# Performance work log

Measured on AMD Instinct MI355X. Metric: run time of the kernel, lower is better.

Reference implementation:

```python
import jax, jax.numpy as jnp
import numpy as np
from jax import lax

B = 8192      # batch (many parallel RL envs)
E = 16        # token_embed_size
IE = 128      # image_embed_size == semi_memory_size == LSTM hidden
H = 128       # text GRU hidden (text_embedding_size)
W_EMB = 32    # word_embedding_size
T = 20        # text length
V = 100       # text vocab (obs_space['text'])
NACT = 7      # action_space.n
EMB = IE + H  # embedding_size = 256


def setup_inputs() -> dict:
    key = jax.random.key(0)
    ks = jax.random.split(key, 32)
    f = lambda k, shape, s=0.1: (jax.random.normal(k, shape, jnp.float32) * s)
    C1 = IE // 2
    return {
        'image': jax.random.randint(ks[0], (B, 7, 7, 3), 0, 2),
        'memory': jax.random.normal(ks[1], (B, 2 * IE), jnp.float32),
        'text': jax.random.randint(ks[2], (B, T), 0, V),
        'obj_emb': f(ks[3], (11, E)),
        'col_emb': f(ks[4], (6, E)),
        'st_emb': f(ks[5], (2, E)),
        'conv1_w': f(ks[6], (C1, 3 * E, 2, 2)), 'conv1_b': jnp.zeros((C1,), jnp.float32),
        'conv2_w': f(ks[7], (C1, C1, 2, 2)), 'conv2_b': jnp.zeros((C1,), jnp.float32),
        'conv3_w': f(ks[8], (IE, C1, 2, 2)), 'conv3_b': jnp.zeros((IE,), jnp.float32),
        'lstm_wih': f(ks[9], (4 * IE, IE)), 'lstm_whh': f(ks[10], (4 * IE, IE)),
        'lstm_bih': jnp.zeros((4 * IE,), jnp.float32), 'lstm_bhh': jnp.zeros((4 * IE,), jnp.float32),
        'word_emb': f(ks[11], (V, W_EMB)),
        'gru_wih': f(ks[12], (3 * H, W_EMB)), 'gru_whh': f(ks[13], (3 * H, H)),
        'gru_bih': jnp.zeros((3 * H,), jnp.float32), 'gru_bhh': jnp.zeros((3 * H,), jnp.float32),
        'actor_w1': f(ks[14], (EMB, EMB)), 'actor_b1': jnp.zeros((EMB,), jnp.float32),
        'actor_w2': f(ks[15], (NACT, EMB)), 'actor_b2': jnp.zeros((NACT,), jnp.float32),
        'critic_w1': f(ks[16], (EMB, EMB)), 'critic_b1': jnp.zeros((EMB,), jnp.float32),
        'critic_w2': f(ks[17], (1, EMB)), 'critic_b2': jnp.zeros((1,), jnp.float32),
    }


def reference(image, memory, text, obj_emb, col_emb, st_emb,
              conv1_w, conv1_b, conv2_w, conv2_b, conv3_w, conv3_b,
              lstm_wih, lstm_whh, lstm_bih, lstm_bhh,
              word_emb, gru_wih, gru_whh, gru_bih, gru_bhh,
              actor_w1, actor_b1, actor_w2, actor_b2,
              critic_w1, critic_b1, critic_w2, critic_b2):
    Hs = lstm_whh.shape[1]
    # embed + concat (color, object, state) on last dim, then NHWC->NCHW
    im = jnp.concatenate([col_emb[image[..., 1]], obj_emb[image[..., 0]], st_emb[image[..., 2]]], axis=3)
    x = jnp.transpose(im, (0, 3, 1, 2))  # [B, 3E, 7, 7]
    dn = ('NCHW', 'OIHW', 'NCHW')
    conv = lambda x, w, b: lax.conv_general_dilated(x, w, (1, 1), 'VALID', dimension_numbers=dn) + b[None, :, None, None]
    x = jax.nn.relu(conv(x, conv1_w, conv1_b))                                 # [B, 64, 6, 6]
    x = lax.reduce_window(x, -jnp.inf, lax.max, (1, 1, 2, 2), (1, 1, 2, 2), 'VALID')  # [B, 64, 3, 3]
    x = jax.nn.relu(conv(x, conv2_w, conv2_b))                                 # [B, 64, 2, 2]
    x = jax.nn.relu(conv(x, conv3_w, conv3_b))                                 # [B, 128, 1, 1]
    x = x.reshape(x.shape[0], -1)
    # LSTMCell (torch gate order i, f, g, o)
    h, c = memory[:, :Hs], memory[:, Hs:]
    gates = x @ lstm_wih.T + lstm_bih + h @ lstm_whh.T + lstm_bhh
    i, f, g, o = jnp.split(gates, 4, axis=1)
    c = jax.nn.sigmoid(f) * c + jax.nn.sigmoid(i) * jnp.tanh(g)
    h = jax.nn.sigmoid(o) * jnp.tanh(c)
    memory_out = jnp.concatenate([h, c], axis=1)
    # text GRU (torch gate order r, z, n); precompute input-side gates
    wemb = word_emb[text]  # [B, T, 32]
    gi_all = jnp.einsum('btd,gd->btg', wemb, gru_wih) + gru_bih  # [B, T, 3H]
    HH = gru_whh.shape[1]
    def step(ht, gi):
        gh = ht @ gru_whh.T + gru_bhh
        r = jax.nn.sigmoid(gi[:, :HH] + gh[:, :HH])
        z = jax.nn.sigmoid(gi[:, HH:2 * HH] + gh[:, HH:2 * HH])
        n = jnp.tanh(gi[:, 2 * HH:] + r * gh[:, 2 * HH:])
        return (1.0 - z) * n + z * ht, None
    h0 = jnp.zeros((wemb.shape[0], HH), wemb.dtype)
    ht, _ = lax.scan(step, h0, jnp.swapaxes(gi_all, 0, 1))
    emb = jnp.concatenate([h, ht], axis=1)  # [B, 256]
    logits = jnp.tanh(emb @ actor_w1.T + actor_b1) @ actor_w2.T + actor_b2
    log_probs = jax.nn.log_softmax(logits, axis=1)  # Categorical logits
    value = (jnp.tanh(emb @ critic_w1.T + critic_b1) @ critic_w2.T + critic_b2)[:, 0]
    return (log_probs, value, memory_out)
```

## Files before the change

kernel.cpp:

```cpp
#include <hip/hip_runtime.h>

#define Bsz   8192
#define Tlen  20
#define OUT_VAL_OFF  57344
#define OUT_MEM_OFF  65536

#define WS_GI     0
#define WS_D1     153600
#define WS_WT     161792
#define WS_WHF    686080
#define WS_WTBH   882688
#define WS_WTBL   1144832
#define WS_LB     1406976
#define WS_C2W    1409024
#define WS_C2B    1474560
#define WS_C3W    1474816
#define WS_C3B    1605888
#define WS_C1B    1606400
#define WS_BH     1606656
#define WS_B1     1608192
#define WS_W2     1610240
#define WS_B2     1618432
#define WS_FLAG   1618464
#define WS_WHB    1618496
#define WS_LWTB   1716800

#define GBLK   512
#define GROWS  16
#define PREP_TASKS 404616

using frag16 = __attribute__((ext_vector_type(8))) short;
using fragf4 = __attribute__((ext_vector_type(4))) float;

__device__ __forceinline__ float bf2f(unsigned short u){
    union { unsigned int i; float f; } v; v.i = ((unsigned int)u) << 16; return v.f;
}
__device__ __forceinline__ unsigned short f2bf(float f){
    union { float f; unsigned int i; } v; v.f = f;
    unsigned int x = v.i;
    return (unsigned short)((x + 0x7fffu + ((x >> 16) & 1u)) >> 16);
}
__device__ __forceinline__ float sigm(float x){ return 1.0f / (1.0f + __expf(-x)); }
__device__ __forceinline__ float tanh_f(float x){ return 1.0f - 2.0f / (__expf(2.0f * x) + 1.0f); }

template<bool BF>
__device__ __forceinline__ float G(const void* p, int i){
    if (BF) return bf2f(((const unsigned short*)p)[i]);
    else    return ((const float*)p)[i];
}

__global__ __launch_bounds__(256) void sniff_kernel(
    const unsigned short* __restrict__ we, int* __restrict__ flag)
{
    __shared__ int cnt;
    if (threadIdx.x == 0) cnt = 0;
    __syncthreads();
    int c = 0;
    for (int i = threadIdx.x; i < 2048; i += 256) {
        int e = (we[i] >> 7) & 0xFF;
        if (e >= 96 && e <= 160) c++;
    }
    atomicAdd(&cnt, c);
    __syncthreads();
    if (threadIdx.x == 0) *flag = (cnt >= 1792) ? 1 : 0;
}

template<bool BF>
__global__ __launch_bounds__(256) void prep_kernel(
    const int* __restrict__ flag,
    const void* word_emb, const void* gru_wih, const void* gru_bih,
    const void* col_emb, const void* obj_emb, const void* st_emb,
    const void* conv1_w, const void* conv1_b,
    const void* conv2_w, const void* conv2_b,
    const void* conv3_w, const void* conv3_b,
    const void* lstm_wih, const void* lstm_whh,
    const void* lstm_bih, const void* lstm_bhh,
    const void* actor_w1, const void* actor_b1,
    const void* actor_w2, const void* actor_b2,
    const void* critic_w1, const void* critic_b1,
    const void* critic_w2, const void* critic_b2,
    const void* gru_whh, const void* gru_bhh,
    float* __restrict__ ws0)
{
    if ((*flag != 0) != BF) return;
    int task = blockIdx.x * 256 + threadIdx.x;
    if (task >= PREP_TASKS) return;
    char* wsb = (char*)ws0;
    if (task < 38400) {
        int v = task / 384, g = task - v * 384;
        float acc = G<BF>(gru_bih, g);
        #pragma unroll
        for (int d = 0; d < 32; d++)
            acc += G<BF>(word_emb, v * 32 + d) * G<BF>(gru_wih, g * 32 + d);
        ((float*)(wsb + WS_GI))[task] = acc;
    } else if (task < 40448) {
        int i2 = task - 38400;
        int o = i2 & 63; int tkk = i2 >> 6;
        int kx = tkk & 1, ky = (tkk >> 1) & 1, t = tkk >> 2;
        int c = t & 1, ob = (t >> 1) & 1, s = (t >> 2) & 1;
        float acc = 0.f;
        #pragma unroll
        for (int i = 0; i < 48; i++) {
            float e;
            if (i < 16)      e = G<BF>(col_emb, c * 16 + i);
            else if (i < 32) e = G<BF>(obj_emb, ob * 16 + (i - 16));
            else             e = G<BF>(st_emb, s * 16 + (i - 32));
            acc += e * G<BF>(conv1_w, ((o * 48 + i) * 2 + ky) * 2 + kx);
        }
        ((float*)(wsb + WS_D1))[tkk * 64 + ((o + tkk) & 63)] = acc;
    } else if (task < 171520) {
        int i3 = task - 40448;
        int u = i3 >> 8, k = i3 & 255;
        float w = (u < 256) ? G<BF>(actor_w1, u * 256 + k)
                            : G<BF>(critic_w1, (u - 256) * 256 + k);
        unsigned short hi = f2bf(w);
        ((unsigned short*)(wsb + WS_WTBH))[i3] = hi;
        ((unsigned short*)(wsb + WS_WTBL))[i3] = f2bf(w - bf2f(hi));
    } else if (task < 172032) {
        int i = task - 171520;
        ((float*)(wsb + WS_LB))[i] = G<BF>(lstm_bih, i) + G<BF>(lstm_bhh, i);
    } else if (task < 188416) {
        int i = task - 172032;
        int o = i & 63, pp = (i >> 6) & 3, ii = i >> 8;
        ((float*)(wsb + WS_C2W))[i] = G<BF>(conv2_w, o * 256 + ii * 4 + pp);
    } else if (task < 188480) {
        int i = task - 188416;
        ((float*)(wsb + WS_C2B))[i] = G<BF>(conv2_b, i);
    } else if (task < 221248) {
        int i = task - 188480;
        int o = i & 127, kk = i >> 7;
        ((float*)(wsb + WS_C3W))[i] = G<BF>(conv3_w, o * 256 + kk);
    } else if (task < 221376) {
        int i = task - 221248;
        ((float*)(wsb + WS_C3B))[i] = G<BF>(conv3_b, i);
    } else if (task < 221440) {
        int i = task - 221376;
        ((float*)(wsb + WS_C1B))[i] = G<BF>(conv1_b, i);
    } else if (task < 221824) {
        int i = task - 221440;
        ((float*)(wsb + WS_BH))[i] = G<BF>(gru_bhh, i);
    } else if (task < 222336) {
        int i = task - 221824;
        ((float*)(wsb + WS_B1))[i] = (i < 256) ? G<BF>(actor_b1, i) : G<BF>(critic_b1, i - 256);
    } else if (task < 224384) {
        int i = task - 222336;
        int u = i >> 8, k = i & 255;
        ((float*)(wsb + WS_W2))[i] = (u < 7) ? G<BF>(actor_w2, u * 256 + k) : G<BF>(critic_w2, k);
    } else if (task < 224392) {
        int i = task - 224384;
        ((float*)(wsb + WS_B2))[i] = (i < 7) ? G<BF>(actor_b2, i) : G<BF>(critic_b2, 0);
    } else if (task < 273544) {
        int i = task - 224392;
        ((unsigned short*)(wsb + WS_WHB))[i] = f2bf(G<BF>(gru_whh, i));
    } else {
        int i = task - 273544;
        int g = i >> 8, k = i & 255;
        float v = (k < 128) ? G<BF>(lstm_wih, g * 128 + k)
                            : G<BF>(lstm_whh, g * 128 + (k - 128));
        ((unsigned short*)(wsb + WS_LWTB))[i] = f2bf(v);
    }
}

__global__ __launch_bounds__(256) void conv_kernel(
    const int* __restrict__ image,
    const float* __restrict__ ws0,
    float* __restrict__ mem_out)
{
    const char* wsb = (const char*)ws0;
    const float* D1g  = (const float*)(wsb + WS_D1);
    const float* c1bF = (const float*)(wsb + WS_C1B);
    const float* c2wT = (const float*)(wsb + WS_C2W);
    const float* c2bF = (const float*)(wsb + WS_C2B);
    const float* c3wT = (const float*)(wsb + WS_C3W);
    const float* c3bF = (const float*)(wsb + WS_C3B);

    __shared__ __align__(16) float sp1[576 * 8];
    __shared__ __align__(16) float sp2[256 * 9];
    __shared__ __align__(16) float sD1[2048];
    __shared__ unsigned char stt[392];

    int tid = threadIdx.x;
    int b0 = blockIdx.x * 8;

    for (int i = tid; i < 2048; i += 256) sD1[i] = D1g[i];
    for (int i = tid; i < 392; i += 256) {
        int s = i / 49, p = i - s * 49;
        int base = ((b0 + s) * 49 + p) * 3;
        stt[i] = (unsigned char)(image[base + 1] | (image[base] << 1) | (image[base + 2] << 2));
    }
    __syncthreads();

    for (int task = tid; task < 4608; task += 256) {
        int s = task & 7;
        int op = task >> 3;
        int o = op / 9, p = op - o * 9;
        int py = p / 3, px = p - py * 3;
        float bo = c1bF[o];
        float mx = 0.f;
        #pragma unroll
        for (int dy = 0; dy < 2; dy++)
        #pragma unroll
        for (int dx = 0; dx < 2; dx++) {
            int y = 2 * py + dy, x = 2 * px + dx;
            float sum = bo;
            #pragma unroll
            for (int ky = 0; ky < 2; ky++)
            #pragma unroll
            for (int kx = 0; kx < 2; kx++) {
                int t = stt[s * 49 + (y + ky) * 7 + (x + kx)];
                int tkk = t * 4 + ky * 2 + kx;
                sum += sD1[tkk * 64 + ((o + tkk) & 63)];
            }
            mx = fmaxf(mx, sum);
        }
        sp1[op * 8 + s] = mx;
    }
    __syncthreads();

    {
        int ot = tid & 63, st4 = tid >> 6;
        int s0 = st4 * 2;
        float b = c2bF[ot];
        float acc[4][2];
        #pragma unroll
        for (int p = 0; p < 4; p++) { acc[p][0] = b; acc[p][1] = b; }
        for (int i = 0; i < 64; i++) {
            float w0 = c2wT[(i * 4 + 0) * 64 + ot];
            float w1 = c2wT[(i * 4 + 1) * 64 + ot];
            float w2 = c2wT[(i * 4 + 2) * 64 + ot];
            float w3 = c2wT[(i * 4 + 3) * 64 + ot];
            #pragma unroll
            for (int ss = 0; ss < 2; ss++) {
                const float* vr = sp1 + i * 72 + s0 + ss;
                float v0 = vr[0],  v1 = vr[8],  v2 = vr[16];
                float v3 = vr[24], v4 = vr[32], v5 = vr[40];
                float v6 = vr[48], v7 = vr[56], v8 = vr[64];
                acc[0][ss] += w0 * v0 + w1 * v1 + w2 * v3 + w3 * v4;
                acc[1][ss] += w0 * v1 + w1 * v2 + w2 * v4 + w3 * v5;
                acc[2][ss] += w0 * v3 + w1 * v4 + w2 * v6 + w3 * v7;
                acc[3][ss] += w0 * v4 + w1 * v5 + w2 * v7 + w3 * v8;
            }
        }
        int key = ot >> 3;
        #pragma unroll
        for (int p = 0; p < 4; p++)
            #pragma unroll
            for (int ss = 0; ss < 2; ss++)
                sp2[(ot * 4 + p) * 9 + ((s0 + ss + key) & 7)] = fmaxf(acc[p][ss], 0.f);
    }
    __syncthreads();

    {
        int ot = tid & 127, st2 = tid >> 7;
        int s0 = st2 * 4;
        float b = c3bF[ot];
        float acc[4] = { b, b, b, b };
        for (int kk = 0; kk < 256; kk++) {
            float w = c3wT[kk * 128 + ot];
            const float* ar = sp2 + kk * 9;
            int sw = (kk >> 5) & 7;
            acc[0] = fmaf(w, ar[(s0 + 0 + sw) & 7], acc[0]);
            acc[1] = fmaf(w, ar[(s0 + 1 + sw) & 7], acc[1]);
            acc[2] = fmaf(w, ar[(s0 + 2 + sw) & 7], acc[2]);
            acc[3] = fmaf(w, ar[(s0 + 3 + sw) & 7], acc[3]);
        }
        #pragma unroll
        for (int ss = 0; ss < 4; ss++)
            mem_out[(b0 + s0 + ss) * 256 + ot] = fmaxf(acc[ss], 0.f);
    }
}

#define GI_LOAD(dst, t) do {                                                  \
    _Pragma("unroll")                                                         \
    for (int rg_ = 0; rg_ < 4; rg_++) {                                       \
        int tok_ = sTok2[(m0 + rg_) * Tlen + (t)];                            \
        const float* gp_ = gi_table + tok_ * 384 + j;                         \
        dst[rg_ * 3 + 0] = gp_[0];                                            \
        dst[rg_ * 3 + 1] = gp_[128];                                          \
        dst[rg_ * 3 + 2] = gp_[256];                                          \
    }                                                                         \
} while (0)

#define GRU_STEP(SRD, SWR, GC, GN, T) do {                                    \
    frag16 Af_[4];                                                            \
    _Pragma("unroll")                                                         \
    for (int kc_ = 0; kc_ < 4; kc_++)                                         \
        Af_[kc_] = *(const frag16*)((SRD) + l16 * 136 + kc_ * 32 + quad * 8); \
    fragf4 aR_ = {0.f,0.f,0.f,0.f}, aZ_ = {0.f,0.f,0.f,0.f};                  \
    fragf4 aN_ = {0.f,0.f,0.f,0.f};                                           \
    _Pragma("unroll")                                                         \
    for (int kc_ = 0; kc_ < 4; kc_++) {                                       \
        aR_ = __builtin_amdgcn_mfma_f32_16x16x32_bf16(Af_[kc_], Bf0[kc_], aR_, 0, 0, 0); \
        aZ_ = __builtin_amdgcn_mfma_f32_16x16x32_bf16(Af_[kc_], Bf1[kc_], aZ_, 0, 0, 0); \
        aN_ = __builtin_amdgcn_mfma_f32_16x16x32_bf16(Af_[kc_], Bf2[kc_], aN_, 0, 0, 0); \
    }                                                                         \
    if ((T) < Tlen - 1) GI_LOAD(GN, (T) + 1);                                 \
    _Pragma("unroll")                                                         \
    for (int reg_ = 0; reg_ < 4; reg_++) {                                    \
        float rg2_ = sigm(GC[reg_*3+0] + aR_[reg_] + bh0);                    \
        float zg_  = sigm(GC[reg_*3+1] + aZ_[reg_] + bh1);                    \
        float ng_  = tanh_f(GC[reg_*3+2] + rg2_ * (aN_[reg_] + bh2));         \
        float hn_  = (1.f - zg_) * ng_ + zg_ * hpv[reg_];                     \
        unsigned short hb_ = f2bf(hn_);                                       \
        hpv[reg_] = bf2f(hb_);                                                \
        (SWR)[(m0 + reg_) * 136 + j] = hb_;                                   \
    }                                                                         \
    __syncthreads();                                                          \
} while (0)

__global__ __launch_bounds__(512, 4) void gru_head_kernel(
    const int* __restrict__ flag,
    const int* __restrict__ text, const void* memory,
    const float* __restrict__ ws0,
    float* __restrict__ mem_out,
    float* __restrict__ out_lp, float* __restrict__ out_val)
{
    const char* wsb = (const char*)ws0;
    const unsigned short* whb2 = (const unsigned short*)(wsb + WS_WHB);
    const unsigned short* lwtb = (const unsigned short*)(wsb + WS_LWTB);
    const unsigned short* wtbh = (const unsigned short*)(wsb + WS_WTBH);
    const unsigned short* wtbl = (const unsigned short*)(wsb + WS_WTBL);
    const float* gi_table = (const float*)(wsb + WS_GI);
    const float* bhF      = (const float*)(wsb + WS_BH);
    const float* b1F      = (const float*)(wsb + WS_B1);
    const float* W2f      = (const float*)(wsb + WS_W2);
    const float* B2f      = (const float*)(wsb + WS_B2);
    const float* lbF      = (const float*)(wsb + WS_LB);

    __shared__ __align__(16) char sU[25600];
    __shared__ float sScore[64];
    __shared__ int   sTok2[320];

    unsigned short* sEh  = (unsigned short*)sU;
    unsigned short* sEl  = (unsigned short*)(sU + 8448);
    unsigned short* sHtA = (unsigned short*)(sU + 16896);
    unsigned short* sHtB = (unsigned short*)(sU + 21248);
    float* sHid = (float*)sU;

    int tid = threadIdx.x;
    int rbase = blockIdx.x * GROWS;
    int wave = tid >> 6, lane = tid & 63;
    int quad = lane >> 4, l16 = lane & 15;
    int j = wave * 16 + l16;
    int m0 = quad * 4;
    const bool bfin = (*flag != 0);
    const unsigned short* mem16 = (const unsigned short*)memory;
    const float*          memf  = (const float*)memory;

    for (int i = tid; i < 4096; i += 512) {
        int m = i >> 8, k = i & 255;
        float v;
        if (k < 128) v = mem_out[(rbase + m) * 256 + k];
        else v = bfin ? bf2f(mem16[(rbase + m) * 256 + (k - 128)])
                      : memf[(rbase + m) * 256 + (k - 128)];
        sEh[m * 264 + k] = f2bf(v);
    }
    for (int i = tid; i < 2176; i += 512) sHtA[i] = 0;
    if (tid < 320) sTok2[tid] = text[rbase * Tlen + tid];
    __syncthreads();

    {
        frag16 Ax[8];
        #pragma unroll
        for (int kc = 0; kc < 8; kc++)
            Ax[kc] = *(const frag16*)(sEh + l16 * 264 + kc * 32 + quad * 8);
        fragf4 aI = {0.f,0.f,0.f,0.f}, aF = {0.f,0.f,0.f,0.f};
        fragf4 aG = {0.f,0.f,0.f,0.f}, aO = {0.f,0.f,0.f,0.f};
        #pragma unroll
        for (int kc = 0; kc < 8; kc++) {
            int ko = kc * 32 + quad * 8;
            frag16 bI = *(const frag16*)(lwtb + (j)       * 256 + ko);
            frag16 bF = *(const frag16*)(lwtb + (128 + j) * 256 + ko);
            frag16 bG = *(const frag16*)(lwtb + (256 + j) * 256 + ko);
            frag16 bO = *(const frag16*)(lwtb + (384 + j) * 256 + ko);
            aI = __builtin_amdgcn_mfma_f32_16x16x32_bf16(Ax[kc], bI, aI, 0, 0, 0);
            aF = __builtin_amdgcn_mfma_f32_16x16x32_bf16(Ax[kc], bF, aF, 0, 0, 0);
            aG = __builtin_amdgcn_mfma_f32_16x16x32_bf16(Ax[kc], bG, aG, 0, 0, 0);
            aO = __builtin_amdgcn_mfma_f32_16x16x32_bf16(Ax[kc], bO, aO, 0, 0, 0);
        }
        float lbI = lbF[j], lbFg = lbF[128 + j], lbG = lbF[256 + j], lbO = lbF[384 + j];
        __syncthreads();
        #pragma unroll
        for (int reg = 0; reg < 4; reg++) {
            int m = m0 + reg;
            float ig = sigm(aI[reg] + lbI);
            float fg = sigm(aF[reg] + lbFg);
            float gv = tanh_f(aG[reg] + lbG);
            float og = sigm(aO[reg] + lbO);
            float cv = bfin ? bf2f(mem16[(rbase + m) * 256 + 128 + j])
                            : memf[(rbase + m) * 256 + 128 + j];
            float cn = fg * cv + ig * gv;
            float hn = og * tanh_f(cn);
            mem_out[(rbase + m) * 256 + j]       = hn;
            mem_out[(rbase + m) * 256 + 128 + j] = cn;
            unsigned short hh = f2bf(hn);
            sEh[m * 264 + j] = hh;
            sEl[m * 264 + j] = f2bf(hn - bf2f(hh));
        }
    }

    frag16 Bf0[4], Bf1[4], Bf2[4];
    #pragma unroll
    for (int kc = 0; kc < 4; kc++) {
        int ko = kc * 32 + quad * 8;
        Bf0[kc] = *(const frag16*)(whb2 + (j)       * 128 + ko);
        Bf1[kc] = *(const frag16*)(whb2 + (128 + j) * 128 + ko);
        Bf2[kc] = *(const frag16*)(whb2 + (256 + j) * 128 + ko);
    }
    float bh0 = bhF[j], bh1 = bhF[128 + j], bh2 = bhF[256 + j];
    float hpv[4] = { 0.f, 0.f, 0.f, 0.f };
    float ga[12], gb[12];

    GI_LOAD(ga, 0);

    for (int tt = 0; tt < 10; tt++) {
        int t0 = tt * 2;
        GRU_STEP(sHtA, sHtB, ga, gb, t0);
        GRU_STEP(sHtB, sHtA, gb, ga, t0 + 1);
    }

    #pragma unroll
    for (int reg = 0; reg < 4; reg++) {
        int m = m0 + reg;
        sEh[m * 264 + 128 + j] = f2bf(hpv[reg]);
    }
    __syncthreads();

    fragf4 acc[4];
    {
        fragf4 z4 = {0.f,0.f,0.f,0.f};
        #pragma unroll
        for (int jb = 0; jb < 4; jb++) acc[jb] = z4;
        #pragma unroll
        for (int kc = 0; kc < 8; kc++) {
            int ko = kc * 32 + quad * 8;
            frag16 Eh = *(const frag16*)(sEh + l16 * 264 + ko);
            #pragma unroll
            for (int jb = 0; jb < 4; jb++) {
                int u = jb * 128 + wave * 16 + l16;
                frag16 Wh = *(const frag16*)(wtbh + u * 256 + ko);
                frag16 Wl = *(const frag16*)(wtbl + u * 256 + ko);
                acc[jb] = __builtin_amdgcn_mfma_f32_16x16x32_bf16(Eh, Wh, acc[jb], 0, 0, 0);
                acc[jb] = __builtin_amdgcn_mfma_f32_16x16x32_bf16(Eh, Wl, acc[jb], 0, 0, 0);
            }
            if (kc < 4) {
                frag16 El = *(const frag16*)(sEl + l16 * 264 + ko);
                #pragma unroll
                for (int jb = 0; jb < 4; jb++) {
                    int u = jb * 128 + wave * 16 + l16;
                    frag16 Wh = *(const frag16*)(wtbh + u * 256 + ko);
                    acc[jb] = __builtin_amdgcn_mfma_f32_16x16x32_bf16(El, Wh, acc[jb], 0, 0, 0);
                }
            }
        }
    }
    __syncthreads();

    #pragma unroll
    for (int half = 0; half < 2; half++) {
        if ((quad >> 1) == half) {
            #pragma unroll
            for (int jb = 0; jb < 4; jb++) {
                int u = jb * 128 + wave * 16 + l16;
                float bu = b1F[u];
                #pragma unroll
                for (int reg = 0; reg < 4; reg++) {
                    int mm = (m0 & 7) + reg;
                    sHid[u * 8 + ((mm + (u & 7)) & 7)] = tanh_f(acc[jb][reg] + bu);
                }
            }
        }
        __syncthreads();
        float acc2 = 0.f;
        int r = tid >> 3, i = tid & 7;
        if (tid < 64) {
            acc2 = B2f[i];
            const float* wrp = W2f + i * 256;
            int ubase = (i < 7) ? 0 : 256;
            for (int k = 0; k < 256; k++) {
                int u = ubase + k;
                acc2 += wrp[k] * sHid[u * 8 + ((r + (u & 7)) & 7)];
            }
            sScore[tid] = acc2;
        }
        __syncthreads();
        if (tid < 64) {
            const float* sr = sScore + r * 8;
            float mx = sr[0];
            #pragma unroll
            for (int a = 1; a < 7; a++) mx = fmaxf(mx, sr[a]);
            float se = 0.f;
            #pragma unroll
            for (int a = 0; a < 7; a++) se += __expf(sr[a] - mx);
            float lse = mx + __logf(se);
            int row = rbase + half * 8 + r;
            if (i < 7) out_lp[row * 7 + i] = acc2 - lse;
            else       out_val[row] = acc2;
        }
        if (half == 0) __syncthreads();
    }
}

extern "C" void kernel_launch(void* const* d_in, const int* in_sizes, int n_in,
                              void* d_out, int out_size, void* d_ws, size_t ws_size,
                              hipStream_t stream) {
    const int*  image  = (const int*)d_in[0];
    const void* memory = d_in[1];
    const int*  text   = (const int*)d_in[2];

    char* wsb = (char*)d_ws;
    float* ws0  = (float*)wsb;
    int*   flag = (int*)(wsb + WS_FLAG);

    float* out = (float*)d_out;
    float* out_lp  = out;
    float* out_val = out + OUT_VAL_OFF;
    float* mem_out = out + OUT_MEM_OFF;

    sniff_kernel<<<1, 256, 0, stream>>>((const unsigned short*)d_in[16], flag);

    const int PREP_GRID = (PREP_TASKS + 255) / 256;
    prep_kernel<true><<<PREP_GRID, 256, 0, stream>>>(flag,
        d_in[16], d_in[17], d_in[19], d_in[4], d_in[3], d_in[5],
        d_in[6], d_in[7], d_in[8], d_in[9], d_in[10], d_in[11],
        d_in[12], d_in[13], d_in[14], d_in[15],
        d_in[21], d_in[22], d_in[23], d_in[24],
        d_in[25], d_in[26], d_in[27], d_in[28],
        d_in[18], d_in[20], ws0);
    prep_kernel<false><<<PREP_GRID, 256, 0, stream>>>(flag,
        d_in[16], d_in[17], d_in[19], d_in[4], d_in[3], d_in[5],
        d_in[6], d_in[7], d_in[8], d_in[9], d_in[10], d_in[11],
        d_in[12], d_in[13], d_in[14], d_in[15],
        d_in[21], d_in[22], d_in[23], d_in[24],
        d_in[25], d_in[26], d_in[27], d_in[28],
        d_in[18], d_in[20], ws0);

    conv_kernel<<<Bsz / 8, 256, 0, stream>>>(image, ws0, mem_out);

    gru_head_kernel<<<GBLK, 512, 0, stream>>>(flag, text, memory, ws0,
                                              mem_out, out_lp, out_val);
}
```

Baseline: 279.9 us.

## Move conv2 and conv3 to bf16x3 split-precision MFMA

Conv2 and conv3 in the conv kernel now run on MFMA 16x16x32 bf16 instructions instead of scalar FP32 FMA loops. Activations and weights are split into high and low bf16 parts, and three MFMAs per tile keep accuracy close to FP32. A prep step writes the split weights into the workspace. The conv stages should become much cheaper, but the kernel does more MFMAs than a plain bf16 version and conv3 leaves half its M tile idle because there are only 8 samples per block.

Measured after the change: 266.9 us. 4.6% less time.

```diff
diff --git a/kernel.cpp b/kernel.cpp
--- a/kernel.cpp
+++ b/kernel.cpp
@@ -7,7 +7,10 @@
 
 #define WS_GI     0
 #define WS_D1     153600
-#define WS_WT     161792
+#define WS_W2BH   161792
+#define WS_W2BL   194560
+#define WS_W3BH   227328
+#define WS_W3BL   292864
 #define WS_WHF    686080
 #define WS_WTBH   882688
 #define WS_WTBL   1144832
@@ -27,7 +30,7 @@
 
 #define GBLK   512
 #define GROWS  16
-#define PREP_TASKS 404616
+#define PREP_TASKS 453768
 
 using frag16 = __attribute__((ext_vector_type(8))) short;
 using fragf4 = __attribute__((ext_vector_type(4))) float;
@@ -39,6 +42,12 @@
     union { float f; unsigned int i; } v; v.f = f;
     unsigned int x = v.i;
     return (unsigned short)((x + 0x7fffu + ((x >> 16) & 1u)) >> 16);
+}
+__device__ __forceinline__ void f2bf2(float f, unsigned short &h, unsigned short &l){
+    union { float f; unsigned int i; } u; u.f = f;
+    h = (unsigned short)(u.i >> 16);
+    union { unsigned int i; float f; } t; t.i = u.i & 0xffff0000u;
+    l = f2bf(f - t.f);
 }
 __device__ __forceinline__ float sigm(float x){ return 1.0f / (1.0f + __expf(-x)); }
 __device__ __forceinline__ float tanh_f(float x){ return 1.0f - 2.0f / (__expf(2.0f * x) + 1.0f); }
@@ -152,12 +161,24 @@
     } else if (task < 273544) {
         int i = task - 224392;
         ((unsigned short*)(wsb + WS_WHB))[i] = f2bf(G<BF>(gru_whh, i));
-    } else {
+    } else if (task < 404616) {
         int i = task - 273544;
         int g = i >> 8, k = i & 255;
         float v = (k < 128) ? G<BF>(lstm_wih, g * 128 + k)
                             : G<BF>(lstm_whh, g * 128 + (k - 128));
         ((unsigned short*)(wsb + WS_LWTB))[i] = f2bf(v);
+    } else if (task < 421000) {
+        int i = task - 404616;
+        float w = G<BF>(conv2_w, i);
+        unsigned short hi = f2bf(w);
+        ((unsigned short*)(wsb + WS_W2BH))[i] = hi;
+        ((unsigned short*)(wsb + WS_W2BL))[i] = f2bf(w - bf2f(hi));
+    } else {
+        int i = task - 421000;
+        float w = G<BF>(conv3_w, i);
+        unsigned short hi = f2bf(w);
+        ((unsigned short*)(wsb + WS_W3BH))[i] = hi;
+        ((unsigned short*)(wsb + WS_W3BL))[i] = f2bf(w - bf2f(hi));
     }
 }
 
@@ -169,18 +190,24 @@
     const char* wsb = (const char*)ws0;
     const float* D1g  = (const float*)(wsb + WS_D1);
     const float* c1bF = (const float*)(wsb + WS_C1B);
-    const float* c2wT = (const float*)(wsb + WS_C2W);
     const float* c2bF = (const float*)(wsb + WS_C2B);
-    const float* c3wT = (const float*)(wsb + WS_C3W);
     const float* c3bF = (const float*)(wsb + WS_C3B);
-
-    __shared__ __align__(16) float sp1[576 * 8];
-    __shared__ __align__(16) float sp2[256 * 9];
+    const unsigned short* w2bh = (const unsigned short*)(wsb + WS_W2BH);
+    const unsigned short* w2bl = (const unsigned short*)(wsb + WS_W2BL);
+    const unsigned short* w3bh = (const unsigned short*)(wsb + WS_W3BH);
+    const unsigned short* w3bl = (const unsigned short*)(wsb + WS_W3BL);
+
+    __shared__ __align__(16) unsigned short sp1h[4608];
+    __shared__ __align__(16) unsigned short sp1l[4608];
+    __shared__ __align__(16) unsigned short sA3h[9 * 264];
+    __shared__ __align__(16) unsigned short sA3l[9 * 264];
     __shared__ __align__(16) float sD1[2048];
     __shared__ unsigned char stt[392];
 
     int tid = threadIdx.x;
     int b0 = blockIdx.x * 8;
+    int wave = tid >> 6, lane = tid & 63;
+    int quad = lane >> 4, l16 = lane & 15;
 
     for (int i = tid; i < 2048; i += 256) sD1[i] = D1g[i];
     for (int i = tid; i < 392; i += 256) {
@@ -188,6 +215,7 @@
         int base = ((b0 + s) * 49 + p) * 3;
         stt[i] = (unsigned char)(image[base + 1] | (image[base] << 1) | (image[base + 2] << 2));
     }
+    for (int i = tid; i < 264; i += 256) { sA3h[8 * 264 + i] = 0; sA3l[8 * 264 + i] = 0; }
     __syncthreads();
 
     for (int task = tid; task < 4608; task += 256) {
@@ -213,60 +241,101 @@
             }
             mx = fmaxf(mx, sum);
         }
-        sp1[op * 8 + s] = mx;
+        unsigned short h, l;
+        f2bf2(mx, h, l);
+        sp1h[op * 8 + s] = h;
+        sp1l[op * 8 + s] = l;
     }
     __syncthreads();
 
     {
-        int ot = tid & 63, st4 = tid >> 6;
-        int s0 = st4 * 2;
-        float b = c2bF[ot];
-        float acc[4][2];
-        #pragma unroll
-        for (int p = 0; p < 4; p++) { acc[p][0] = b; acc[p][1] = b; }
-        for (int i = 0; i < 64; i++) {
-            float w0 = c2wT[(i * 4 + 0) * 64 + ot];
-            float w1 = c2wT[(i * 4 + 1) * 64 + ot];
-            float w2 = c2wT[(i * 4 + 2) * 64 + ot];
-            float w3 = c2wT[(i * 4 + 3) * 64 + ot];
-            #pragma unroll
-            for (int ss = 0; ss < 2; ss++) {
-                const float* vr = sp1 + i * 72 + s0 + ss;
-                float v0 = vr[0],  v1 = vr[8],  v2 = vr[16];
-                float v3 = vr[24], v4 = vr[32], v5 = vr[40];
-                float v6 = vr[48], v7 = vr[56], v8 = vr[64];
-                acc[0][ss] += w0 * v0 + w1 * v1 + w2 * v3 + w3 * v4;
-                acc[1][ss] += w0 * v1 + w1 * v2 + w2 * v4 + w3 * v5;
-                acc[2][ss] += w0 * v3 + w1 * v4 + w2 * v6 + w3 * v7;
-                acc[3][ss] += w0 * v4 + w1 * v5 + w2 * v7 + w3 * v8;
+        int Mt  = wave >> 1;
+        int NtB = (wave & 1) * 2;
+        int s_a = Mt * 4 + (l16 >> 2);
+        int p2  = l16 & 3;
+        int bp  = 3 * (p2 >> 1) + (p2 & 1);
+        fragf4 acc0 = {0.f,0.f,0.f,0.f}, acc1 = {0.f,0.f,0.f,0.f};
+        int u0 = (NtB * 16 + l16) * 256;
+        int u1 = u0 + 16 * 256;
+        #pragma unroll
+        for (int kc = 0; kc < 8; kc++) {
+            int k0 = kc * 32 + quad * 8;
+            int i0 = k0 >> 2;
+            const unsigned short* hp = sp1h + (i0 * 9 + bp) * 8 + s_a;
+            const unsigned short* lp = sp1l + (i0 * 9 + bp) * 8 + s_a;
+            frag16 Ah, Al;
+            Ah[0] = (short)hp[0];  Ah[1] = (short)hp[8];
+            Ah[2] = (short)hp[24]; Ah[3] = (short)hp[32];
+            Ah[4] = (short)hp[72]; Ah[5] = (short)hp[80];
+            Ah[6] = (short)hp[96]; Ah[7] = (short)hp[104];
+            Al[0] = (short)lp[0];  Al[1] = (short)lp[8];
+            Al[2] = (short)lp[24]; Al[3] = (short)lp[32];
+            Al[4] = (short)lp[72]; Al[5] = (short)lp[80];
+            Al[6] = (short)lp[96]; Al[7] = (short)lp[104];
+            frag16 W0h = *(const frag16*)(w2bh + u0 + k0);
+            frag16 W0l = *(const frag16*)(w2bl + u0 + k0);
+            frag16 W1h = *(const frag16*)(w2bh + u1 + k0);
+            frag16 W1l = *(const frag16*)(w2bl + u1 + k0);
+            acc0 = __builtin_amdgcn_mfma_f32_16x16x32_bf16(Ah, W0h, acc0, 0, 0, 0);
+            acc0 = __builtin_amdgcn_mfma_f32_16x16x32_bf16(Al, W0h, acc0, 0, 0, 0);
+            acc0 = __builtin_amdgcn_mfma_f32_16x16x32_bf16(Ah, W0l, acc0, 0, 0, 0);
+            acc1 = __builtin_amdgcn_mfma_f32_16x16x32_bf16(Ah, W1h, acc1, 0, 0, 0);
+            acc1 = __builtin_amdgcn_mfma_f32_16x16x32_bf16(Al, W1h, acc1, 0, 0, 0);
+            acc1 = __builtin_amdgcn_mfma_f32_16x16x32_bf16(Ah, W1l, acc1, 0, 0, 0);
+        }
+        int sC = Mt * 4 + quad;
+        #pragma unroll
+        for (int nt = 0; nt < 2; nt++) {
+            fragf4 a = nt ? acc1 : acc0;
+            int o2 = (NtB + nt) * 16 + l16;
+            float b = c2bF[o2];
+            #pragma unroll
+            for (int reg = 0; reg < 4; reg++) {
+                float v = fmaxf(a[reg] + b, 0.f);
+                unsigned short h, l;
+                f2bf2(v, h, l);
+                sA3h[sC * 264 + o2 * 4 + reg] = h;
+                sA3l[sC * 264 + o2 * 4 + reg] = l;
             }
         }
-        int key = ot >> 3;
-        #pragma unroll
-        for (int p = 0; p < 4; p++)
-            #pragma unroll
-            for (int ss = 0; ss < 2; ss++)
-                sp2[(ot * 4 + p) * 9 + ((s0 + ss + key) & 7)] = fmaxf(acc[p][ss], 0.f);
     }
     __syncthreads();
 
     {
-        int ot = tid & 127, st2 = tid >> 7;
-        int s0 = st2 * 4;
-        float b = c3bF[ot];
-        float acc[4] = { b, b, b, b };
-        for (int kk = 0; kk < 256; kk++) {
-            float w = c3wT[kk * 128 + ot];
-            const float* ar = sp2 + kk * 9;
-            int sw = (kk >> 5) & 7;
-            acc[0] = fmaf(w, ar[(s0 + 0 + sw) & 7], acc[0]);
-            acc[1] = fmaf(w, ar[(s0 + 1 + sw) & 7], acc[1]);
-            acc[2] = fmaf(w, ar[(s0 + 2 + sw) & 7], acc[2]);
-            acc[3] = fmaf(w, ar[(s0 + 3 + sw) & 7], acc[3]);
-        }
-        #pragma unroll
-        for (int ss = 0; ss < 4; ss++)
-            mem_out[(b0 + s0 + ss) * 256 + ot] = fmaxf(acc[ss], 0.f);
+        int NtB = wave * 2;
+        int s_a = (l16 < 8) ? l16 : 8;
+        fragf4 acc0 = {0.f,0.f,0.f,0.f}, acc1 = {0.f,0.f,0.f,0.f};
+        int u0 = (NtB * 16 + l16) * 256;
+        int u1 = u0 + 16 * 256;
+        #pragma unroll
+        for (int kc = 0; kc < 8; kc++) {
+            int k0 = kc * 32 + quad * 8;
+            frag16 Ah = *(const frag16*)(sA3h + s_a * 264 + k0);
+            frag16 Al = *(const frag16*)(sA3l + s_a * 264 + k0);
+            frag16 W0h = *(const frag16*)(w3bh + u0 + k0);
+            frag16 W0l = *(const frag16*)(w3bl + u0 + k0);
+            frag16 W1h = *(const frag16*)(w3bh + u1 + k0);
+            frag16 W1l = *(const frag16*)(w3bl + u1 + k0);
+            acc0 = __builtin_amdgcn_mfma_f32_16x16x32_bf16(Ah, W0h, acc0, 0, 0, 0);
+            acc0 = __builtin_amdgcn_mfma_f32_16x16x32_bf16(Al, W0h, acc0, 0, 0, 0);
+            acc0 = __builtin_amdgcn_mfma_f32_16x16x32_bf16(Ah, W0l, acc0, 0, 0, 0);
+            acc1 = __builtin_amdgcn_mfma_f32_16x16x32_bf16(Ah, W1h, acc1, 0, 0, 0);
+            acc1 = __builtin_amdgcn_mfma_f32_16x16x32_bf16(Al, W1h, acc1, 0, 0, 0);
+            acc1 = __builtin_amdgcn_mfma_f32_16x16x32_bf16(Ah, W1l, acc1, 0, 0, 0);
+        }
+        if (quad < 2) {
+            #pragma unroll
+            for (int nt = 0; nt < 2; nt++) {
+                fragf4 a = nt ? acc1 : acc0;
+                int o3 = (NtB + nt) * 16 + l16;
+                float b = c3bF[o3];
+                #pragma unroll
+                for (int reg = 0; reg < 4; reg++) {
+                    int s = quad * 4 + reg;
+                    mem_out[(b0 + s) * 256 + o3] = fmaxf(a[reg] + b, 0.f);
+                }
+            }
+        }
     }
 }
 
```
